# Kernel tuning notes

Measured on AMD Instinct MI355X. Metric: run time of the kernel, lower is better.

Reference implementation:

```python
import jax, jax.numpy as jnp
import numpy as np

B, N = 64, 4096
D_IN, D_SLOT, K, N_ITER, MLP_H = 128, 128, 8, 3, 256
EPS = 1e-8
LN_EPS = 1e-5  # torch LayerNorm default


def layer_norm(x, g, b):
    m = jnp.mean(x, axis=-1, keepdims=True)
    v = jnp.mean((x - m) ** 2, axis=-1, keepdims=True)
    return (x - m) * jax.lax.rsqrt(v + LN_EPS) * g + b


def setup_inputs() -> dict:
    key = jax.random.key(0)
    ks = jax.random.split(key, 12)
    s = D_SLOT ** -0.5
    return {
        "inputs": jax.random.normal(ks[0], (B, N, D_IN), jnp.float32),
        "noise": jax.random.normal(ks[1], (B, K, D_SLOT), jnp.float32),
        "ln_in_g": jnp.ones((D_IN,), jnp.float32),
        "ln_in_b": jnp.zeros((D_IN,), jnp.float32),
        "ln_sl_g": jnp.ones((D_SLOT,), jnp.float32),
        "ln_sl_b": jnp.zeros((D_SLOT,), jnp.float32),
        "ln_mlp_g": jnp.ones((D_SLOT,), jnp.float32),
        "ln_mlp_b": jnp.zeros((D_SLOT,), jnp.float32),
        "slots_mu": jax.random.normal(ks[2], (1, 1, D_SLOT), jnp.float32) * s,
        "slots_log_sigma": jnp.zeros((1, 1, D_SLOT), jnp.float32),
        "Wq": jax.random.normal(ks[3], (D_SLOT, D_SLOT), jnp.float32) * s,
        "Wk": jax.random.normal(ks[4], (D_SLOT, D_IN), jnp.float32) * s,
        "Wv": jax.random.normal(ks[5], (D_SLOT, D_IN), jnp.float32) * s,
        "gru_Wih": jax.random.normal(ks[6], (3 * D_SLOT, D_SLOT), jnp.float32) * s,
        "gru_Whh": jax.random.normal(ks[7], (3 * D_SLOT, D_SLOT), jnp.float32) * s,
        "gru_bih": jnp.zeros((3 * D_SLOT,), jnp.float32),
        "gru_bhh": jnp.zeros((3 * D_SLOT,), jnp.float32),
        "mlp_W1": jax.random.normal(ks[8], (MLP_H, D_SLOT), jnp.float32) * s,
        "mlp_b1": jnp.zeros((MLP_H,), jnp.float32),
        "mlp_W2": jax.random.normal(ks[9], (D_SLOT, MLP_H), jnp.float32) * (MLP_H ** -0.5),
        "mlp_b2": jnp.zeros((D_SLOT,), jnp.float32),
    }


def gru_cell(x, h, Wih, Whh, bih, bhh):
    # torch GRUCell: gate order r, z, n
    gx = x @ Wih.T + bih
    gh = h @ Whh.T + bhh
    xr, xz, xn = jnp.split(gx, 3, axis=-1)
    hr, hz, hn = jnp.split(gh, 3, axis=-1)
    r = jax.nn.sigmoid(xr + hr)
    z = jax.nn.sigmoid(xz + hz)
    n = jnp.tanh(xn + r * hn)
    return (1.0 - z) * n + z * h


def reference(inputs, noise, ln_in_g, ln_in_b, ln_sl_g, ln_sl_b, ln_mlp_g, ln_mlp_b,
              slots_mu, slots_log_sigma, Wq, Wk, Wv,
              gru_Wih, gru_Whh, gru_bih, gru_bhh,
              mlp_W1, mlp_b1, mlp_W2, mlp_b2):
    # init slots: mu + sigma * eps
    slots = slots_mu + jnp.exp(slots_log_sigma) * noise  # (B, K, d)
    x = layer_norm(inputs, ln_in_g, ln_in_b)
    k = jnp.einsum('bnd,ed->bne', x, Wk)  # (B, N, d_slot)
    v = jnp.einsum('bnd,ed->bne', x, Wv)
    scale = D_SLOT ** -0.5
    attn = None
    for _ in range(N_ITER):
        slots_prev = slots
        s_n = layer_norm(slots, ln_sl_g, ln_sl_b)
        q = jnp.einsum('bkd,ed->bke', s_n, Wq)
        dots = jnp.einsum('bkd,bnd->bkn', q, k) * scale
        attn = jax.nn.softmax(dots, axis=1)  # competitive: softmax over slots
        attn_normed = attn / (jnp.sum(attn, axis=-1, keepdims=True) + EPS)
        updates = jnp.einsum('bkn,bnd->bkd', attn_normed, v)
        slots = gru_cell(updates.reshape(-1, D_SLOT), slots_prev.reshape(-1, D_SLOT),
                         gru_Wih, gru_Whh, gru_bih, gru_bhh).reshape(B, K, D_SLOT)
        h = layer_norm(slots, ln_mlp_g, ln_mlp_b)
        h = jax.nn.gelu(h @ mlp_W1.T + mlp_b1, approximate=False)
        slots = slots + h @ mlp_W2.T + mlp_b2
    return slots, attn
```

## Files before the change

### kernel.cpp

```cpp
#include <hip/hip_runtime.h>
#include <hip/hip_bf16.h>
#include <math.h>

typedef unsigned int u32;
typedef unsigned long long u64;
typedef unsigned short u16;
typedef __bf16 bf16x8 __attribute__((ext_vector_type(8)));
typedef float f32x4 __attribute__((ext_vector_type(4)));

#define DEV __device__ __forceinline__

DEV u32 bfr(float f){ u32 u = __float_as_uint(f); return (u + 0x7fffu + ((u>>16)&1u)) >> 16; }
DEV u16 b1v(float a){ return __builtin_bit_cast(u16, (__bf16)a); }
DEV u32 pk2(float a, float b){
  return (u32)__builtin_bit_cast(u16, (__bf16)a) | ((u32)__builtin_bit_cast(u16, (__bf16)b) << 16);
}
DEV float red32(float v){
  v += __shfl_xor(v,1); v += __shfl_xor(v,2); v += __shfl_xor(v,4);
  v += __shfl_xor(v,8); v += __shfl_xor(v,16); return v;
}

__global__ void kInitSlots(const float* __restrict__ noise, const float* __restrict__ mu,
                           const float* __restrict__ ls, float* __restrict__ slots){
  int i4 = blockIdx.x*256 + threadIdx.x;
  int d4 = i4 & 31;
  float4 nv = ((const float4*)noise)[i4];
  float4 mv = ((const float4*)mu)[d4];
  float4 lv = ((const float4*)ls)[d4];
  float4 r;
  r.x = mv.x + expf(lv.x)*nv.x;
  r.y = mv.y + expf(lv.y)*nv.y;
  r.z = mv.z + expf(lv.z)*nv.z;
  r.w = mv.w + expf(lv.w)*nv.w;
  ((float4*)slots)[i4] = r;
}

__global__ void kInitW(const float* __restrict__ Wk, const float* __restrict__ Wv,
                       const float* __restrict__ g, const float* __restrict__ bb,
                       u16* __restrict__ wg, float* __restrict__ c1, float* __restrict__ c2){
  int e = threadIdx.x;
  const float4* src = (const float4*)((e < 128) ? (Wk + e*128) : (Wv + (e-128)*128));
  float a1 = 0.f, a2 = 0.f;
  #pragma unroll
  for (int d4 = 0; d4 < 32; ++d4){
    float4 wv = src[d4];
    float4 gv = ((const float4*)g)[d4];
    float4 bv = ((const float4*)bb)[d4];
    a1 += wv.x*gv.x + wv.y*gv.y + wv.z*gv.z + wv.w*gv.w;
    a2 += wv.x*bv.x + wv.y*bv.y + wv.z*bv.z + wv.w*bv.w;
    u32 w0 = bfr(wv.x*gv.x) | (bfr(wv.y*gv.y) << 16);
    u32 w1 = bfr(wv.z*gv.z) | (bfr(wv.w*gv.w) << 16);
    *(uint2*)&wg[e*128 + d4*4] = make_uint2(w0, w1);
  }
  c1[e] = a1; c2[e] = a2;
}

__global__ void kInitT(const float* __restrict__ Wih, const float* __restrict__ Whh,
                       const float* __restrict__ W1, const float* __restrict__ W2,
                       float2* __restrict__ gruT, float* __restrict__ w1T, float* __restrict__ w2T){
  int i = blockIdx.x*256 + threadIdx.x;
  if (i < 49152){
    int d = i / 384, g = i - d*384;
    gruT[i] = make_float2(Wih[g*128 + d], Whh[g*128 + d]);
  } else if (i < 81920){
    int j = i - 49152;
    int d = j >> 8, h = j & 255;
    w1T[j] = W1[h*128 + d];
  } else if (i < 114688){
    int q = i - 81920;
    int j = q >> 7, d = q & 127;
    w2T[q] = W2[d*256 + j];
  }
}

__global__ __launch_bounds__(512, 2) void kA(const float* __restrict__ x,
    const u16* __restrict__ wg, const float* __restrict__ c1g, const float* __restrict__ c2g,
    u16* __restrict__ kbuf, u16* __restrict__ vbuf)
{
  __shared__ __align__(16) u16 sWg[128*128];
  __shared__ __align__(16) u16 sE[8*16*128];
  __shared__ float sC1[128], sC2[128];
  const int t = threadIdx.x, l = t & 63, w = t >> 6;
  const int bid = blockIdx.x;
  const int half = (bid >> 3) & 1;
  const int rowgroup = (bid & 7)*32 + (bid >> 4);
  const int rowbase = rowgroup * 1024;

  const uint4* wg4 = (const uint4*)wg;
  #pragma unroll
  for (int p = 0; p < 4; ++p){
    int G = t + p*512;
    int row = G >> 4, g = G & 15;
    uint4 v = wg4[(half*128 + row)*16 + g];
    *(uint4*)&sWg[row*128 + ((g ^ (row & 7)) << 3)] = v;
  }
  if (t < 128){ sC1[t] = c1g[half*128 + t]; sC2[t] = c2g[half*128 + t]; }
  __syncthreads();

  u16* dstbuf = half ? vbuf : kbuf;
  const float4* x4 = (const float4*)x;

  #pragma unroll 1
  for (int s = 0; s < 8; ++s){
    const int r0 = rowbase + s*128 + w*16;
    const int myrow = r0 + (l & 15);
    float s1 = 0.f, s2 = 0.f;
    uint4 af[4];
    #pragma unroll
    for (int kt = 0; kt < 4; ++kt){
      int g = kt*4 + (l >> 4);
      float4 A = x4[(size_t)myrow*32 + g*2];
      float4 B = x4[(size_t)myrow*32 + g*2 + 1];
      s1 += A.x + A.y + A.z + A.w + B.x + B.y + B.z + B.w;
      s2 += A.x*A.x + A.y*A.y + A.z*A.z + A.w*A.w
          + B.x*B.x + B.y*B.y + B.z*B.z + B.w*B.w;
      af[kt].x = pk2(A.x, A.y);
      af[kt].y = pk2(A.z, A.w);
      af[kt].z = pk2(B.x, B.y);
      af[kt].w = pk2(B.z, B.w);
    }
    s1 += __shfl_xor(s1, 16); s2 += __shfl_xor(s2, 16);
    s1 += __shfl_xor(s1, 32); s2 += __shfl_xor(s2, 32);
    float m = s1 * 0.0078125f;
    float rstd = rsqrtf(s2 * 0.0078125f - m*m + 1e-5f);
    f32x4 acc[8];
    #pragma unroll
    for (int c_ = 0; c_ < 8; ++c_) acc[c_] = (f32x4){0.f,0.f,0.f,0.f};
    #pragma unroll
    for (int ct = 0; ct < 8; ++ct){
      uint4 bf[4];
      #pragma unroll
      for (int kt = 0; kt < 4; ++kt){
        int wr = ct*16 + (l & 15);
        int g = kt*4 + (l >> 4);
        bf[kt] = *(const uint4*)&sWg[wr*128 + ((g ^ (wr & 7)) << 3)];
      }
      #pragma unroll
      for (int kt = 0; kt < 4; ++kt)
        acc[ct] = __builtin_amdgcn_mfma_f32_16x16x32_bf16(
            __builtin_bit_cast(bf16x8, af[kt]),
            __builtin_bit_cast(bf16x8, bf[kt]),
            acc[ct], 0, 0, 0);
    }
    float mvp[4], rvp[4];
    #pragma unroll
    for (int r = 0; r < 4; ++r){
      int rl = (l >> 4)*4 + r;
      mvp[r] = __shfl(m, rl);
      rvp[r] = __shfl(rstd, rl);
    }
    #pragma unroll
    for (int ct = 0; ct < 8; ++ct){
      int col = ct*16 + (l & 15);
      float c1v = sC1[col], c2v = sC2[col];
      #pragma unroll
      for (int r = 0; r < 4; ++r){
        int rl = (l >> 4)*4 + r;
        float valf = rvp[r]*(acc[ct][r] - mvp[r]*c1v) + c2v;
        int gran = (col >> 3) ^ (rl & 7);
        sE[w*2048 + rl*128 + (gran << 3) + (col & 7)] = b1v(valf);
      }
    }
    uint4* dst4 = (uint4*)dstbuf;
    #pragma unroll
    for (int p = 0; p < 4; ++p){
      int fl = l + p*64;
      int nl = fl >> 4, gb = fl & 15;
      uint4 v = *(const uint4*)&sE[w*2048 + nl*128 + ((gb ^ (nl & 7)) << 3)];
      dst4[(size_t)(r0 + nl)*16 + gb] = v;
    }
  }
}

__global__ __launch_bounds__(256) void kB(const float* __restrict__ slots,
   const u16* __restrict__ kbuf, const u16* __restrict__ vbuf,
   const float* __restrict__ Wq, const float* __restrict__ lng, const float* __restrict__ lnb,
   float* __restrict__ part, float* __restrict__ attn_out, int write_attn)
{
  const int t = threadIdx.x;
  const int b = blockIdx.x >> 3, chunk = blockIdx.x & 7;
  const int w = t >> 6, l = t & 63;
  const int k8 = t >> 5, q32 = t & 31;
  __shared__ __align__(16) float sSn[8*128];
  __shared__ __align__(16) float sQ[8*128];
  __shared__ __align__(16) u16 sVT[128*64];
  __shared__ __align__(16) u16 sAttnB[16*64];
  __shared__ float sRsP[32];

  {
    float4 sv = ((const float4*)slots)[b*256 + t];
    float s  = sv.x + sv.y + sv.z + sv.w;
    float ss = sv.x*sv.x + sv.y*sv.y + sv.z*sv.z + sv.w*sv.w;
    s = red32(s); ss = red32(ss);
    float m = s*0.0078125f, var = ss*0.0078125f - m*m;
    float rstd = rsqrtf(var + 1e-5f);
    float4 gv = ((const float4*)lng)[q32], bv = ((const float4*)lnb)[q32];
    float4 sn;
    sn.x = (sv.x - m)*rstd*gv.x + bv.x;
    sn.y = (sv.y - m)*rstd*gv.y + bv.y;
    sn.z = (sv.z - m)*rstd*gv.z + bv.z;
    sn.w = (sv.w - m)*rstd*gv.w + bv.w;
    *(float4*)&sSn[t*4] = sn;
  }
  __syncthreads();
  {
    const float4* Wq4 = (const float4*)Wq;
    #pragma unroll
    for (int i = 0; i < 4; ++i){
      int e = i*32 + q32;
      float acc = 0.f;
      #pragma unroll
      for (int d4 = 0; d4 < 32; ++d4){
        float4 qs = *(const float4*)&sSn[k8*128 + d4*4];
        float4 wv = Wq4[e*32 + d4];
        acc = fmaf(qs.x,wv.x,acc); acc = fmaf(qs.y,wv.y,acc);
        acc = fmaf(qs.z,wv.z,acc); acc = fmaf(qs.w,wv.w,acc);
      }
      sQ[k8*128 + e] = acc * 0.08838834764831845f;
    }
  }
  __syncthreads();

  uint4 qf[4];
  {
    int slot = l & 15;
    #pragma unroll
    for (int kt = 0; kt < 4; ++kt){
      uint4 z = make_uint4(0,0,0,0);
      if (slot < 8){
        int e0 = kt*32 + (l >> 4)*8;
        float4 qa = *(const float4*)&sQ[slot*128 + e0];
        float4 qb = *(const float4*)&sQ[slot*128 + e0 + 4];
        z.x = pk2(qa.x, qa.y); z.y = pk2(qa.z, qa.w);
        z.z = pk2(qb.x, qb.y); z.w = pk2(qb.z, qb.w);
      }
      qf[kt] = z;
    }
  }

  f32x4 accPV0 = (f32x4){0.f,0.f,0.f,0.f};
  f32x4 accPV1 = (f32x4){0.f,0.f,0.f,0.f};
  float rs = 0.f;
  const int myrow = w*16 + (l & 15);
  const size_t base = (size_t)b*4096 + (size_t)chunk*512;

  uint4 kf[4];
  {
    const u16* kr = kbuf + (base + myrow)*128;
    #pragma unroll
    for (int kt = 0; kt < 4; ++kt) kf[kt] = *(const uint4*)(kr + (kt*4 + (l>>4))*8);
  }

  #pragma unroll 1
  for (int tile = 0; tile < 8; ++tile){
    const int n0 = tile*64;
    uint4 vld[4];
    {
      const uint4* vg = (const uint4*)(vbuf + (base + n0)*128);
      #pragma unroll
      for (int p = 0; p < 4; ++p) vld[p] = vg[t + p*256];
    }
    f32x4 dacc = (f32x4){0.f,0.f,0.f,0.f};
    #pragma unroll
    for (int kt = 0; kt < 4; ++kt)
      dacc = __builtin_amdgcn_mfma_f32_16x16x32_bf16(
          __builtin_bit_cast(bf16x8, kf[kt]),
          __builtin_bit_cast(bf16x8, qf[kt]), dacc, 0, 0, 0);
    if (tile < 7){
      const u16* kr = kbuf + (base + n0 + 64 + myrow)*128;
      #pragma unroll
      for (int kt = 0; kt < 4; ++kt) kf[kt] = *(const uint4*)(kr + (kt*4 + (l>>4))*8);
    }
    float at[4];
    #pragma unroll
    for (int r = 0; r < 4; ++r){
      float d = dacc[r];
      float mx = fmaxf(d, __shfl_xor(d, 1));
      mx = fmaxf(mx, __shfl_xor(mx, 2));
      mx = fmaxf(mx, __shfl_xor(mx, 4));
      float e = expf(d - mx);
      float s = e + __shfl_xor(e, 1);
      s += __shfl_xor(s, 2);
      s += __shfl_xor(s, 4);
      at[r] = e / s;
      rs += at[r];
    }
    {
      int slot = l & 15;
      int nb = w*16 + (l >> 4)*4;
      u32 lo = pk2(at[0], at[1]), hi = pk2(at[2], at[3]);
      int g = (nb >> 3) ^ (slot & 7);
      *(u64*)((char*)sAttnB + slot*128 + (g << 4) + ((nb & 7) << 1)) = ((u64)hi << 32) | (u64)lo;
    }
    #pragma unroll
    for (int p = 0; p < 4; ++p){
      int fl = t + p*256;
      int nl = fl >> 4, gb = fl & 15;
      u32 arr[4] = {vld[p].x, vld[p].y, vld[p].z, vld[p].w};
      #pragma unroll
      for (int h = 0; h < 4; ++h){
        #pragma unroll
        for (int e2 = 0; e2 < 2; ++e2){
          int e = h*2 + e2;
          int d = gb*8 + e;
          int g = (nl >> 3) ^ (d & 7) ^ (gb & 7);
          *(u16*)((char*)sVT + d*128 + (g << 4) + ((nl & 7) << 1)) =
              (u16)(e2 ? (arr[h] >> 16) : (arr[h] & 0xffffu));
        }
      }
    }
    __syncthreads();
    #pragma unroll
    for (int step = 0; step < 2; ++step){
      uint4 paf;
      {
        int slot = l & 15;
        int g = (step*4 + (l >> 4)) ^ (slot & 7);
        paf = *(const uint4*)((const char*)sAttnB + slot*128 + (g << 4));
      }
      #pragma unroll
      for (int ct = 0; ct < 2; ++ct){
        int d = w*32 + ct*16 + (l & 15);
        int g = (step*4 + (l >> 4)) ^ (d & 7) ^ ((d >> 3) & 7);
        uint4 pbf = *(const uint4*)((const char*)sVT + d*128 + (g << 4));
        if (ct == 0)
          accPV0 = __builtin_amdgcn_mfma_f32_16x16x32_bf16(
              __builtin_bit_cast(bf16x8, paf), __builtin_bit_cast(bf16x8, pbf), accPV0, 0,0,0);
        else
          accPV1 = __builtin_amdgcn_mfma_f32_16x16x32_bf16(
              __builtin_bit_cast(bf16x8, paf), __builtin_bit_cast(bf16x8, pbf), accPV1, 0,0,0);
      }
    }
    if (write_attn && (l & 15) < 8){
      #pragma unroll
      for (int r = 0; r < 4; ++r)
        attn_out[(size_t)(b*8 + (l & 15))*4096 + chunk*512 + n0 + w*16 + (l >> 4)*4 + r] = at[r];
    }
    __syncthreads();
  }

  float* pb = part + (size_t)blockIdx.x*1040;
  if ((l >> 4) < 2){
    #pragma unroll
    for (int r = 0; r < 4; ++r){
      int slot = (l >> 4)*4 + r;
      pb[slot*128 + w*32 + (l & 15)] = accPV0[r];
      pb[slot*128 + w*32 + 16 + (l & 15)] = accPV1[r];
    }
  }
  rs += __shfl_xor(rs, 16);
  rs += __shfl_xor(rs, 32);
  if (l < 8) sRsP[w*8 + l] = rs;
  __syncthreads();
  if (t < 8) pb[1024 + t] = sRsP[t] + sRsP[8 + t] + sRsP[16 + t] + sRsP[24 + t];
}

__global__ __launch_bounds__(384) void kC(const float* __restrict__ part,
  float* __restrict__ slots, const float2* __restrict__ gruT,
  const float* __restrict__ bih, const float* __restrict__ bhh,
  const float* __restrict__ lng, const float* __restrict__ lnb,
  const float* __restrict__ w1T, const float* __restrict__ b1,
  const float* __restrict__ w2T, const float* __restrict__ b2,
  float* __restrict__ out_slots, int last)
{
  const int t = threadIdx.x;
  const int r = blockIdx.x, b = r >> 3, k = r & 7;
  __shared__ float sU[128], sS[128], sG1[384], sG2[384];
  __shared__ float sNew[128], sH[128], sH1[256];
  __shared__ float sP[4];

  if (t < 128){
    float rs = 1e-8f;
    #pragma unroll
    for (int c = 0; c < 8; ++c) rs += part[(size_t)(b*8 + c)*1040 + 1024 + k];
    float u = 0.f;
    #pragma unroll
    for (int c = 0; c < 8; ++c) u += part[(size_t)(b*8 + c)*1040 + k*128 + t];
    sU[t] = u / rs;
    sS[t] = slots[r*128 + t];
  }
  __syncthreads();

  {
    float acc1 = bih[t], acc2 = bhh[t];
    #pragma unroll 8
    for (int d = 0; d < 128; ++d){
      float2 w = gruT[d*384 + t];
      float ud = sU[d], sd = sS[d];
      acc1 = fmaf(ud, w.x, acc1);
      acc2 = fmaf(sd, w.y, acc2);
    }
    sG1[t] = acc1; sG2[t] = acc2;
  }
  __syncthreads();

  if (t < 128){
    float rr = 1.f/(1.f + expf(-(sG1[t] + sG2[t])));
    float zz = 1.f/(1.f + expf(-(sG1[128 + t] + sG2[128 + t])));
    float nn = tanhf(sG1[256 + t] + rr*sG2[256 + t]);
    sNew[t] = (1.f - zz)*nn + zz*sS[t];
  }
  __syncthreads();
  if (t < 128){
    float v = sNew[t];
    float s = v, ss = v*v;
    s  += __shfl_xor(s,1);  ss += __shfl_xor(ss,1);
    s  += __shfl_xor(s,2);  ss += __shfl_xor(ss,2);
    s  += __shfl_xor(s,4);  ss += __shfl_xor(ss,4);
    s  += __shfl_xor(s,8);  ss += __shfl_xor(ss,8);
    s  += __shfl_xor(s,16); ss += __shfl_xor(ss,16);
    s  += __shfl_xor(s,32); ss += __shfl_xor(ss,32);
    if ((t & 63) == 0){ sP[(t >> 6)*2] = s; sP[(t >> 6)*2 + 1] = ss; }
  }
  __syncthreads();
  if (t < 128){
    float s = sP[0] + sP[2], ss = sP[1] + sP[3];
    float m = s*0.0078125f, var = ss*0.0078125f - m*m;
    float rstd = rsqrtf(var + 1e-5f);
    sH[t] = (sNew[t] - m)*rstd*lng[t] + lnb[t];
  }
  __syncthreads();

  if (t < 256){
    float acc = b1[t];
    #pragma unroll 8
    for (int d = 0; d < 128; ++d)
      acc = fmaf(sH[d], w1T[d*256 + t], acc);
    sH1[t] = 0.5f*acc*(1.f + erff(acc*0.70710678118654752f));
  }
  __syncthreads();

  if (t < 128){
    float acc = b2[t];
    #pragma unroll 8
    for (int j = 0; j < 256; ++j)
      acc = fmaf(sH1[j], w2T[j*128 + t], acc);
    float res = sNew[t] + acc;
    slots[r*128 + t] = res;
    if (last) out_slots[r*128 + t] = res;
  }
}

extern "C" void kernel_launch(void* const* d_in, const int* in_sizes, int n_in,
                              void* d_out, int out_size, void* d_ws, size_t ws_size,
                              hipStream_t stream)
{
  const float* inputs   = (const float*)d_in[0];
  const float* noise    = (const float*)d_in[1];
  const float* ln_in_g  = (const float*)d_in[2];
  const float* ln_in_b  = (const float*)d_in[3];
  const float* ln_sl_g  = (const float*)d_in[4];
  const float* ln_sl_b  = (const float*)d_in[5];
  const float* ln_mlp_g = (const float*)d_in[6];
  const float* ln_mlp_b = (const float*)d_in[7];
  const float* slots_mu = (const float*)d_in[8];
  const float* slots_ls = (const float*)d_in[9];
  const float* Wq  = (const float*)d_in[10];
  const float* Wk  = (const float*)d_in[11];
  const float* Wv  = (const float*)d_in[12];
  const float* Wih = (const float*)d_in[13];
  const float* Whh = (const float*)d_in[14];
  const float* bih = (const float*)d_in[15];
  const float* bhh = (const float*)d_in[16];
  const float* W1  = (const float*)d_in[17];
  const float* b1  = (const float*)d_in[18];
  const float* W2  = (const float*)d_in[19];
  const float* b2  = (const float*)d_in[20];
  float* out = (float*)d_out;

  char* ws = (char*)d_ws;
  u16*   kbuf  = (u16*)ws;
  u16*   vbuf  = (u16*)(ws + 67108864);
  float* slots = (float*)(ws + 134217728);
  u16*   wg    = (u16*)(ws + 134479872);
  float* c1    = (float*)(ws + 134545408);
  float* c2    = (float*)(ws + 134546432);
  float* part  = (float*)(ws + 134547456);
  float2* gruT = (float2*)(ws + 136677376);
  float* w1T   = (float*)(ws + 137070592);
  float* w2T   = (float*)(ws + 137201664);

  kInitSlots<<<64, 256, 0, stream>>>(noise, slots_mu, slots_ls, slots);
  kInitW<<<1, 256, 0, stream>>>(Wk, Wv, ln_in_g, ln_in_b, wg, c1, c2);
  kInitT<<<448, 256, 0, stream>>>(Wih, Whh, W1, W2, gruT, w1T, w2T);
  kA<<<512, 512, 0, stream>>>(inputs, wg, c1, c2, kbuf, vbuf);
  for (int it = 0; it < 3; ++it){
    kB<<<512, 256, 0, stream>>>(slots, kbuf, vbuf, Wq, ln_sl_g, ln_sl_b,
                                part, out + 65536, it == 2);
    kC<<<512, 384, 0, stream>>>(part, slots, gruT, bih, bhh,
                                ln_mlp_g, ln_mlp_b, w1T, b1, w2T, b2, out, it == 2);
  }
}
```

Before: 339.1 us.

## Store V pre-transposed in MFMA fragment layout and drop per-tile LDS transpose

The projection kernel now writes V directly in a blocked, transposed layout that matches the MFMA B-operand fragment, so the attention kernel loads V fragments straight from global memory. This removes the per-tile scalar LDS transpose of V and the block-wide barriers around it. Each wave now covers its own 128-token slice and accumulates all 128 output dims, and the four waves' partials are summed through shared memory at the end. In exchange, each wave holds more accumulator registers and there is an extra reduction step, and K loads are no longer prefetched a tile ahead.

```diff
diff --git a/kernel.cpp b/kernel.cpp
--- a/kernel.cpp
+++ b/kernel.cpp
@@ -97,7 +97,6 @@
   if (t < 128){ sC1[t] = c1g[half*128 + t]; sC2[t] = c2g[half*128 + t]; }
   __syncthreads();
 
-  u16* dstbuf = half ? vbuf : kbuf;
   const float4* x4 = (const float4*)x;
 
   #pragma unroll 1
@@ -149,31 +148,57 @@
       mvp[r] = __shfl(m, rl);
       rvp[r] = __shfl(rstd, rl);
     }
-    #pragma unroll
-    for (int ct = 0; ct < 8; ++ct){
-      int col = ct*16 + (l & 15);
-      float c1v = sC1[col], c2v = sC2[col];
-      #pragma unroll
-      for (int r = 0; r < 4; ++r){
-        int rl = (l >> 4)*4 + r;
-        float valf = rvp[r]*(acc[ct][r] - mvp[r]*c1v) + c2v;
-        int gran = (col >> 3) ^ (rl & 7);
-        sE[w*2048 + rl*128 + (gran << 3) + (col & 7)] = b1v(valf);
-      }
-    }
-    uint4* dst4 = (uint4*)dstbuf;
-    #pragma unroll
-    for (int p = 0; p < 4; ++p){
-      int fl = l + p*64;
-      int nl = fl >> 4, gb = fl & 15;
-      uint4 v = *(const uint4*)&sE[w*2048 + nl*128 + ((gb ^ (nl & 7)) << 3)];
-      dst4[(size_t)(r0 + nl)*16 + gb] = v;
-    }
-  }
-}
-
-__global__ __launch_bounds__(256) void kB(const float* __restrict__ slots,
-   const u16* __restrict__ kbuf, const u16* __restrict__ vbuf,
+    if (half == 0){
+      #pragma unroll
+      for (int ct = 0; ct < 8; ++ct){
+        int col = ct*16 + (l & 15);
+        float c1v = sC1[col], c2v = sC2[col];
+        #pragma unroll
+        for (int r = 0; r < 4; ++r){
+          int rl = (l >> 4)*4 + r;
+          float valf = rvp[r]*(acc[ct][r] - mvp[r]*c1v) + c2v;
+          int gran = (col >> 3) ^ (rl & 7);
+          sE[w*2048 + rl*128 + (gran << 3) + (col & 7)] = b1v(valf);
+        }
+      }
+      uint4* dst4 = (uint4*)kbuf;
+      #pragma unroll
+      for (int p = 0; p < 4; ++p){
+        int fl = l + p*64;
+        int nl = fl >> 4, gb = fl & 15;
+        uint4 v = *(const uint4*)&sE[w*2048 + nl*128 + ((gb ^ (nl & 7)) << 3)];
+        dst4[(size_t)(r0 + nl)*16 + gb] = v;
+      }
+    } else {
+      #pragma unroll
+      for (int ct = 0; ct < 8; ++ct){
+        int col = ct*16 + (l & 15);
+        float c1v = sC1[col], c2v = sC2[col];
+        #pragma unroll
+        for (int r = 0; r < 4; ++r){
+          int nl = (l >> 4)*4 + r;
+          float valf = rvp[r]*(acc[ct][r] - mvp[r]*c1v) + c2v;
+          sE[w*2048 + col*16 + (((nl >> 3) ^ (col & 1)) << 3) + (nl & 7)] = b1v(valf);
+        }
+      }
+      const int bb = rowgroup >> 2;
+      const int nblk = (rowgroup & 3)*32 + s*4 + (w >> 1);
+      uint4* dst4 = (uint4*)vbuf;
+      #pragma unroll
+      for (int p = 0; p < 4; ++p){
+        int u = p*4 + (l >> 4);
+        int dg = u >> 1, no2 = u & 1;
+        int d = dg*16 + (l & 15);
+        uint4 v = *(const uint4*)&sE[w*2048 + d*16 + ((no2 ^ (d & 1)) << 3)];
+        int no = (w & 1)*2 + no2;
+        dst4[((((size_t)bb*8 + dg)*128 + nblk) << 6) + no*16 + (l & 15)] = v;
+      }
+    }
+  }
+}
+
+__global__ __launch_bounds__(256, 2) void kB(const float* __restrict__ slots,
+   const u16* __restrict__ kbuf, const uint4* __restrict__ vT2,
    const float* __restrict__ Wq, const float* __restrict__ lng, const float* __restrict__ lnb,
    float* __restrict__ part, float* __restrict__ attn_out, int write_attn)
 {
@@ -183,9 +208,9 @@
   const int k8 = t >> 5, q32 = t & 31;
   __shared__ __align__(16) float sSn[8*128];
   __shared__ __align__(16) float sQ[8*128];
-  __shared__ __align__(16) u16 sVT[128*64];
-  __shared__ __align__(16) u16 sAttnB[16*64];
-  __shared__ float sRsP[32];
+  __shared__ __align__(16) u16 sAttnB[2048];
+  __shared__ __align__(16) float sRed[4096];
+  __shared__ float sRs[64];
 
   {
     float4 sv = ((const float4*)slots)[b*256 + t];
@@ -238,121 +263,94 @@
     }
   }
 
-  f32x4 accPV0 = (f32x4){0.f,0.f,0.f,0.f};
-  f32x4 accPV1 = (f32x4){0.f,0.f,0.f,0.f};
+  f32x4 accPV[8];
+  #pragma unroll
+  for (int dg = 0; dg < 8; ++dg) accPV[dg] = (f32x4){0.f,0.f,0.f,0.f};
   float rs = 0.f;
-  const int myrow = w*16 + (l & 15);
-  const size_t base = (size_t)b*4096 + (size_t)chunk*512;
-
-  uint4 kf[4];
-  {
-    const u16* kr = kbuf + (base + myrow)*128;
-    #pragma unroll
-    for (int kt = 0; kt < 4; ++kt) kf[kt] = *(const uint4*)(kr + (kt*4 + (l>>4))*8);
-  }
+  const size_t nbase = (size_t)b*4096 + chunk*512 + w*128;
 
   #pragma unroll 1
-  for (int tile = 0; tile < 8; ++tile){
-    const int n0 = tile*64;
-    uint4 vld[4];
-    {
-      const uint4* vg = (const uint4*)(vbuf + (base + n0)*128);
-      #pragma unroll
-      for (int p = 0; p < 4; ++p) vld[p] = vg[t + p*256];
-    }
-    f32x4 dacc = (f32x4){0.f,0.f,0.f,0.f};
-    #pragma unroll
-    for (int kt = 0; kt < 4; ++kt)
-      dacc = __builtin_amdgcn_mfma_f32_16x16x32_bf16(
-          __builtin_bit_cast(bf16x8, kf[kt]),
-          __builtin_bit_cast(bf16x8, qf[kt]), dacc, 0, 0, 0);
-    if (tile < 7){
-      const u16* kr = kbuf + (base + n0 + 64 + myrow)*128;
-      #pragma unroll
-      for (int kt = 0; kt < 4; ++kt) kf[kt] = *(const uint4*)(kr + (kt*4 + (l>>4))*8);
-    }
-    float at[4];
-    #pragma unroll
-    for (int r = 0; r < 4; ++r){
-      float d = dacc[r];
-      float mx = fmaxf(d, __shfl_xor(d, 1));
-      mx = fmaxf(mx, __shfl_xor(mx, 2));
-      mx = fmaxf(mx, __shfl_xor(mx, 4));
-      float e = expf(d - mx);
-      float s = e + __shfl_xor(e, 1);
-      s += __shfl_xor(s, 2);
-      s += __shfl_xor(s, 4);
-      at[r] = e / s;
-      rs += at[r];
-    }
-    {
-      int slot = l & 15;
-      int nb = w*16 + (l >> 4)*4;
-      u32 lo = pk2(at[0], at[1]), hi = pk2(at[2], at[3]);
-      int g = (nb >> 3) ^ (slot & 7);
-      *(u64*)((char*)sAttnB + slot*128 + (g << 4) + ((nb & 7) << 1)) = ((u64)hi << 32) | (u64)lo;
-    }
-    #pragma unroll
-    for (int p = 0; p < 4; ++p){
-      int fl = t + p*256;
-      int nl = fl >> 4, gb = fl & 15;
-      u32 arr[4] = {vld[p].x, vld[p].y, vld[p].z, vld[p].w};
-      #pragma unroll
-      for (int h = 0; h < 4; ++h){
-        #pragma unroll
-        for (int e2 = 0; e2 < 2; ++e2){
-          int e = h*2 + e2;
-          int d = gb*8 + e;
-          int g = (nl >> 3) ^ (d & 7) ^ (gb & 7);
-          *(u16*)((char*)sVT + d*128 + (g << 4) + ((nl & 7) << 1)) =
-              (u16)(e2 ? (arr[h] >> 16) : (arr[h] & 0xffffu));
-        }
-      }
-    }
-    __syncthreads();
-    #pragma unroll
-    for (int step = 0; step < 2; ++step){
-      uint4 paf;
+  for (int t2 = 0; t2 < 4; ++t2){
+    #pragma unroll
+    for (int sub = 0; sub < 2; ++sub){
+      const size_t n0 = nbase + t2*32 + sub*16;
+      const u16* kr = kbuf + (n0 + (l & 15))*128;
+      uint4 kf[4];
+      #pragma unroll
+      for (int kt = 0; kt < 4; ++kt) kf[kt] = *(const uint4*)(kr + (kt*4 + (l >> 4))*8);
+      f32x4 dacc = (f32x4){0.f,0.f,0.f,0.f};
+      #pragma unroll
+      for (int kt = 0; kt < 4; ++kt)
+        dacc = __builtin_amdgcn_mfma_f32_16x16x32_bf16(
+            __builtin_bit_cast(bf16x8, kf[kt]),
+            __builtin_bit_cast(bf16x8, qf[kt]), dacc, 0, 0, 0);
+      float at[4];
+      #pragma unroll
+      for (int r = 0; r < 4; ++r){
+        float d = dacc[r];
+        float mx = fmaxf(d, __shfl_xor(d, 1));
+        mx = fmaxf(mx, __shfl_xor(mx, 2));
+        mx = fmaxf(mx, __shfl_xor(mx, 4));
+        float e = expf(d - mx);
+        float ssum = e + __shfl_xor(e, 1);
+        ssum += __shfl_xor(ssum, 2);
+        ssum += __shfl_xor(ssum, 4);
+        at[r] = e / ssum;
+        rs += at[r];
+      }
       {
         int slot = l & 15;
-        int g = (step*4 + (l >> 4)) ^ (slot & 7);
-        paf = *(const uint4*)((const char*)sAttnB + slot*128 + (g << 4));
-      }
-      #pragma unroll
-      for (int ct = 0; ct < 2; ++ct){
-        int d = w*32 + ct*16 + (l & 15);
-        int g = (step*4 + (l >> 4)) ^ (d & 7) ^ ((d >> 3) & 7);
-        uint4 pbf = *(const uint4*)((const char*)sVT + d*128 + (g << 4));
-        if (ct == 0)
-          accPV0 = __builtin_amdgcn_mfma_f32_16x16x32_bf16(
-              __builtin_bit_cast(bf16x8, paf), __builtin_bit_cast(bf16x8, pbf), accPV0, 0,0,0);
-        else
-          accPV1 = __builtin_amdgcn_mfma_f32_16x16x32_bf16(
-              __builtin_bit_cast(bf16x8, paf), __builtin_bit_cast(bf16x8, pbf), accPV1, 0,0,0);
-      }
-    }
-    if (write_attn && (l & 15) < 8){
-      #pragma unroll
-      for (int r = 0; r < 4; ++r)
-        attn_out[(size_t)(b*8 + (l & 15))*4096 + chunk*512 + n0 + w*16 + (l >> 4)*4 + r] = at[r];
-    }
-    __syncthreads();
-  }
-
-  float* pb = part + (size_t)blockIdx.x*1040;
+        int nl = sub*16 + (l >> 4)*4;
+        int g = (nl >> 3) ^ (slot & 3);
+        *(u64*)((char*)sAttnB + w*1024 + slot*64 + (g << 4) + ((nl & 7) << 1)) =
+            ((u64)pk2(at[2], at[3]) << 32) | (u64)pk2(at[0], at[1]);
+      }
+      if (write_attn && (l & 15) < 8){
+        #pragma unroll
+        for (int r = 0; r < 4; ++r)
+          attn_out[(size_t)(b*8 + (l & 15))*4096 + chunk*512 + w*128 + t2*32 + sub*16 + (l >> 4)*4 + r] = at[r];
+      }
+    }
+    uint4 paf;
+    {
+      int slot = l & 15, q = l >> 4;
+      paf = *(const uint4*)((const char*)sAttnB + w*1024 + slot*64 + ((q ^ (slot & 3)) << 4));
+    }
+    const int nblk = chunk*16 + w*4 + t2;
+    #pragma unroll
+    for (int dg = 0; dg < 8; ++dg){
+      uint4 vf = vT2[((((size_t)b*8 + dg)*128 + nblk) << 6) + l];
+      accPV[dg] = __builtin_amdgcn_mfma_f32_16x16x32_bf16(
+          __builtin_bit_cast(bf16x8, paf),
+          __builtin_bit_cast(bf16x8, vf), accPV[dg], 0, 0, 0);
+    }
+  }
+
   if ((l >> 4) < 2){
     #pragma unroll
-    for (int r = 0; r < 4; ++r){
-      int slot = (l >> 4)*4 + r;
-      pb[slot*128 + w*32 + (l & 15)] = accPV0[r];
-      pb[slot*128 + w*32 + 16 + (l & 15)] = accPV1[r];
-    }
+    for (int dg = 0; dg < 8; ++dg)
+      #pragma unroll
+      for (int r = 0; r < 4; ++r){
+        int slot = (l >> 4)*4 + r;
+        sRed[(slot*128 + dg*16 + (l & 15))*4 + w] = accPV[dg][r];
+      }
   }
   rs += __shfl_xor(rs, 16);
   rs += __shfl_xor(rs, 32);
-  if (l < 8) sRsP[w*8 + l] = rs;
-  __syncthreads();
-  if (t < 8) pb[1024 + t] = sRsP[t] + sRsP[8 + t] + sRsP[16 + t] + sRsP[24 + t];
+  if (l < 16) sRs[w*16 + l] = rs;
+  __syncthreads();
+  float* pb = part + (size_t)blockIdx.x*1040;
+  {
+    float4 o;
+    float* po = &o.x;
+    #pragma unroll
+    for (int j = 0; j < 4; ++j){
+      float4 vv = *(const float4*)&sRed[(t*4 + j)*4];
+      po[j] = vv.x + vv.y + vv.z + vv.w;
+    }
+    *(float4*)&pb[t*4] = o;
+  }
+  if (t < 8) pb[1024 + t] = sRs[t] + sRs[16 + t] + sRs[32 + t] + sRs[48 + t];
 }
 
 __global__ __launch_bounds__(384) void kC(const float* __restrict__ part,
@@ -485,7 +483,7 @@
   kInitT<<<448, 256, 0, stream>>>(Wih, Whh, W1, W2, gruT, w1T, w2T);
   kA<<<512, 512, 0, stream>>>(inputs, wg, c1, c2, kbuf, vbuf);
   for (int it = 0; it < 3; ++it){
-    kB<<<512, 256, 0, stream>>>(slots, kbuf, vbuf, Wq, ln_sl_g, ln_sl_b,
+    kB<<<512, 256, 0, stream>>>(slots, kbuf, (const uint4*)vbuf, Wq, ln_sl_g, ln_sl_b,
                                 part, out + 65536, it == 2);
     kC<<<512, 384, 0, stream>>>(part, slots, gruT, bih, bhh,
                                 ln_mlp_g, ln_mlp_b, w1T, b1, w2T, b2, out, it == 2);
```

New measurement: 442.5 us. +30.5%, slower.

## Hoist slot query projection into separate kernel and split attention into more chunks

Applied to the files above, without the earlier changes.

Moves the slot LayerNorm and Wq projection out of the attention kernel into a small per-batch kernel that writes bf16 query fragments to workspace, so each attention block no longer recomputes the projection. The attention kernel becomes parametric in chunk count and uses 16 chunks of 256 tokens when workspace allows, doubling the grid to 1024 blocks. The aim is to remove redundant projection work per block and raise parallelism across CUs. In exchange it adds an extra kernel launch per iteration and more partial sums for kC to reduce.

```diff
diff --git a/kernel.cpp b/kernel.cpp
--- a/kernel.cpp
+++ b/kernel.cpp
@@ -172,21 +172,14 @@
   }
 }
 
-__global__ __launch_bounds__(256) void kB(const float* __restrict__ slots,
-   const u16* __restrict__ kbuf, const u16* __restrict__ vbuf,
-   const float* __restrict__ Wq, const float* __restrict__ lng, const float* __restrict__ lnb,
-   float* __restrict__ part, float* __restrict__ attn_out, int write_attn)
+__global__ __launch_bounds__(256) void kQ(const float* __restrict__ slots,
+    const float* __restrict__ Wq, const float* __restrict__ lng, const float* __restrict__ lnb,
+    uint4* __restrict__ qg)
 {
-  const int t = threadIdx.x;
-  const int b = blockIdx.x >> 3, chunk = blockIdx.x & 7;
-  const int w = t >> 6, l = t & 63;
+  const int b = blockIdx.x, t = threadIdx.x;
   const int k8 = t >> 5, q32 = t & 31;
-  __shared__ __align__(16) float sSn[8*128];
-  __shared__ __align__(16) float sQ[8*128];
-  __shared__ __align__(16) u16 sVT[128*64];
-  __shared__ __align__(16) u16 sAttnB[16*64];
-  __shared__ float sRsP[32];
-
+  __shared__ __align__(16) float sSn[1024];
+  __shared__ __align__(16) float sQ[1024];
   {
     float4 sv = ((const float4*)slots)[b*256 + t];
     float s  = sv.x + sv.y + sv.z + sv.w;
@@ -220,21 +213,37 @@
     }
   }
   __syncthreads();
+  if (t < 128){
+    int slot = t >> 4, g = t & 15;
+    const float* src = &sQ[slot*128 + g*8];
+    uint4 o;
+    o.x = pk2(src[0], src[1]); o.y = pk2(src[2], src[3]);
+    o.z = pk2(src[4], src[5]); o.w = pk2(src[6], src[7]);
+    qg[(b*8 + slot)*16 + g] = o;
+  }
+}
+
+__global__ __launch_bounds__(256) void kB(const u16* __restrict__ kbuf,
+   const u16* __restrict__ vbuf, const uint4* __restrict__ qg,
+   float* __restrict__ part, float* __restrict__ attn_out, int write_attn,
+   int cshift, int ntiles)
+{
+  const int t = threadIdx.x;
+  const int b = blockIdx.x >> cshift, chunk = blockIdx.x & ((1 << cshift) - 1);
+  const int w = t >> 6, l = t & 63;
+  __shared__ __align__(16) u16 sVT[128*64];
+  __shared__ __align__(16) u16 sAttnB[16*64];
+  __shared__ float sRsP[32];
 
   uint4 qf[4];
   {
     int slot = l & 15;
-    #pragma unroll
-    for (int kt = 0; kt < 4; ++kt){
-      uint4 z = make_uint4(0,0,0,0);
-      if (slot < 8){
-        int e0 = kt*32 + (l >> 4)*8;
-        float4 qa = *(const float4*)&sQ[slot*128 + e0];
-        float4 qb = *(const float4*)&sQ[slot*128 + e0 + 4];
-        z.x = pk2(qa.x, qa.y); z.y = pk2(qa.z, qa.w);
-        z.z = pk2(qb.x, qb.y); z.w = pk2(qb.z, qb.w);
-      }
-      qf[kt] = z;
+    uint4 z = make_uint4(0,0,0,0);
+    qf[0] = z; qf[1] = z; qf[2] = z; qf[3] = z;
+    if (slot < 8){
+      const uint4* qb = qg + ((size_t)b*8 + slot)*16 + (l >> 4);
+      #pragma unroll
+      for (int kt = 0; kt < 4; ++kt) qf[kt] = qb[kt*4];
     }
   }
 
@@ -242,17 +251,17 @@
   f32x4 accPV1 = (f32x4){0.f,0.f,0.f,0.f};
   float rs = 0.f;
   const int myrow = w*16 + (l & 15);
-  const size_t base = (size_t)b*4096 + (size_t)chunk*512;
+  const size_t base = (size_t)b*4096 + (size_t)chunk*(ntiles*64);
 
   uint4 kf[4];
   {
     const u16* kr = kbuf + (base + myrow)*128;
     #pragma unroll
-    for (int kt = 0; kt < 4; ++kt) kf[kt] = *(const uint4*)(kr + (kt*4 + (l>>4))*8);
+    for (int kt = 0; kt < 4; ++kt) kf[kt] = *(const uint4*)(kr + (kt*4 + (l >> 4))*8);
   }
 
   #pragma unroll 1
-  for (int tile = 0; tile < 8; ++tile){
+  for (int tile = 0; tile < ntiles; ++tile){
     const int n0 = tile*64;
     uint4 vld[4];
     {
@@ -266,10 +275,10 @@
       dacc = __builtin_amdgcn_mfma_f32_16x16x32_bf16(
           __builtin_bit_cast(bf16x8, kf[kt]),
           __builtin_bit_cast(bf16x8, qf[kt]), dacc, 0, 0, 0);
-    if (tile < 7){
+    if (tile < ntiles - 1){
       const u16* kr = kbuf + (base + n0 + 64 + myrow)*128;
       #pragma unroll
-      for (int kt = 0; kt < 4; ++kt) kf[kt] = *(const uint4*)(kr + (kt*4 + (l>>4))*8);
+      for (int kt = 0; kt < 4; ++kt) kf[kt] = *(const uint4*)(kr + (kt*4 + (l >> 4))*8);
     }
     float at[4];
     #pragma unroll
@@ -279,18 +288,18 @@
       mx = fmaxf(mx, __shfl_xor(mx, 2));
       mx = fmaxf(mx, __shfl_xor(mx, 4));
       float e = expf(d - mx);
-      float s = e + __shfl_xor(e, 1);
-      s += __shfl_xor(s, 2);
-      s += __shfl_xor(s, 4);
-      at[r] = e / s;
+      float ssum = e + __shfl_xor(e, 1);
+      ssum += __shfl_xor(ssum, 2);
+      ssum += __shfl_xor(ssum, 4);
+      at[r] = e / ssum;
       rs += at[r];
     }
     {
       int slot = l & 15;
       int nb = w*16 + (l >> 4)*4;
-      u32 lo = pk2(at[0], at[1]), hi = pk2(at[2], at[3]);
       int g = (nb >> 3) ^ (slot & 7);
-      *(u64*)((char*)sAttnB + slot*128 + (g << 4) + ((nb & 7) << 1)) = ((u64)hi << 32) | (u64)lo;
+      *(u64*)((char*)sAttnB + slot*128 + (g << 4) + ((nb & 7) << 1)) =
+          ((u64)pk2(at[2], at[3]) << 32) | (u64)pk2(at[0], at[1]);
     }
     #pragma unroll
     for (int p = 0; p < 4; ++p){
@@ -334,7 +343,7 @@
     if (write_attn && (l & 15) < 8){
       #pragma unroll
       for (int r = 0; r < 4; ++r)
-        attn_out[(size_t)(b*8 + (l & 15))*4096 + chunk*512 + n0 + w*16 + (l >> 4)*4 + r] = at[r];
+        attn_out[(size_t)(b*8 + (l & 15))*4096 + chunk*(ntiles*64) + n0 + w*16 + (l >> 4)*4 + r] = at[r];
     }
     __syncthreads();
   }
@@ -361,7 +370,7 @@
   const float* __restrict__ lng, const float* __restrict__ lnb,
   const float* __restrict__ w1T, const float* __restrict__ b1,
   const float* __restrict__ w2T, const float* __restrict__ b2,
-  float* __restrict__ out_slots, int last)
+  float* __restrict__ out_slots, int last, int nchunk)
 {
   const int t = threadIdx.x;
   const int r = blockIdx.x, b = r >> 3, k = r & 7;
@@ -371,11 +380,9 @@
 
   if (t < 128){
     float rs = 1e-8f;
-    #pragma unroll
-    for (int c = 0; c < 8; ++c) rs += part[(size_t)(b*8 + c)*1040 + 1024 + k];
+    for (int c = 0; c < nchunk; ++c) rs += part[(size_t)(b*nchunk + c)*1040 + 1024 + k];
     float u = 0.f;
-    #pragma unroll
-    for (int c = 0; c < 8; ++c) u += part[(size_t)(b*8 + c)*1040 + k*128 + t];
+    for (int c = 0; c < nchunk; ++c) u += part[(size_t)(b*nchunk + c)*1040 + k*128 + t];
     sU[t] = u / rs;
     sS[t] = slots[r*128 + t];
   }
@@ -476,18 +483,29 @@
   float* c1    = (float*)(ws + 134545408);
   float* c2    = (float*)(ws + 134546432);
   float* part  = (float*)(ws + 134547456);
-  float2* gruT = (float2*)(ws + 136677376);
-  float* w1T   = (float*)(ws + 137070592);
-  float* w2T   = (float*)(ws + 137201664);
+
+  int cshift, nchunk;
+  {
+    size_t need16 = 134547456ull + 16ull*64*1040*4 + 393216 + 131072 + 131072 + 131072;
+    if (ws_size >= need16){ cshift = 4; nchunk = 16; }
+    else                  { cshift = 3; nchunk = 8;  }
+  }
+  size_t partB = (size_t)nchunk*64*1040*4;
+  float2* gruT = (float2*)(ws + 134547456 + partB);
+  float*  w1T  = (float*)(ws + 134547456 + partB + 393216);
+  float*  w2T  = (float*)(ws + 134547456 + partB + 393216 + 131072);
+  uint4*  qg   = (uint4*)(ws + 134547456 + partB + 393216 + 262144);
+  int ntiles = 64 / nchunk;
 
   kInitSlots<<<64, 256, 0, stream>>>(noise, slots_mu, slots_ls, slots);
   kInitW<<<1, 256, 0, stream>>>(Wk, Wv, ln_in_g, ln_in_b, wg, c1, c2);
   kInitT<<<448, 256, 0, stream>>>(Wih, Whh, W1, W2, gruT, w1T, w2T);
   kA<<<512, 512, 0, stream>>>(inputs, wg, c1, c2, kbuf, vbuf);
   for (int it = 0; it < 3; ++it){
-    kB<<<512, 256, 0, stream>>>(slots, kbuf, vbuf, Wq, ln_sl_g, ln_sl_b,
-                                part, out + 65536, it == 2);
+    kQ<<<64, 256, 0, stream>>>(slots, Wq, ln_sl_g, ln_sl_b, qg);
+    kB<<<64*nchunk, 256, 0, stream>>>(kbuf, vbuf, qg, part, out + 65536,
+                                      it == 2, cshift, ntiles);
     kC<<<512, 384, 0, stream>>>(part, slots, gruT, bih, bhh,
-                                ln_mlp_g, ln_mlp_b, w1T, b1, w2T, b2, out, it == 2);
-  }
-}
+                                ln_mlp_g, ln_mlp_b, w1T, b1, w2T, b2, out, it == 2, nchunk);
+  }
+}
```

After: 342.1 us. About the same (+0.9%).
